# Kernel optimization log

Measured on AMD Instinct MI355X. Metric: run time of the kernel, lower is better.

Reference implementation:

```python
import jax, jax.numpy as jnp
import numpy as np

IN_FEATURES = 4096
OUT_FEATURES = 11008
IN_GROUP = 8
OUT_GROUP = 1
NUM_CODEBOOKS = 1
CODEBOOK_SIZE = 2 ** 16
NUM_OUT_GROUPS = OUT_FEATURES // OUT_GROUP
NUM_IN_GROUPS = IN_FEATURES // IN_GROUP


def setup_inputs() -> dict:
    key = jax.random.key(0)
    k1, k2, k3, k4, k5 = jax.random.split(key, 5)
    x = jax.random.normal(k1, (4, IN_FEATURES), dtype=jnp.float32)
    codebooks = jax.random.normal(k2, (NUM_CODEBOOKS, CODEBOOK_SIZE, OUT_GROUP, IN_GROUP), dtype=jnp.float32)
    codes = jax.random.randint(k3, (NUM_OUT_GROUPS, NUM_IN_GROUPS, NUM_CODEBOOKS), 0, CODEBOOK_SIZE, dtype=jnp.int32)
    scales = jax.random.uniform(k4, (NUM_OUT_GROUPS, 1, 1, 1), dtype=jnp.float32)
    bias = jax.random.normal(k5, (OUT_FEATURES,), dtype=jnp.float32)
    return {"x": x, "codebooks": codebooks, "codes": codes, "scales": scales, "bias": bias}


def _dequantize_weight(codes, codebooks, scales):
    # codes: [Og, Ig, M] int; codebooks: [M, K, og, ig]; scales: [Og,1,1,1]
    m_idx = jnp.arange(codebooks.shape[0])  # [M]
    # advanced indexing: broadcast [M] with [Og,Ig,M] -> gathered [Og,Ig,M,og,ig]
    gathered = codebooks[m_idx[None, None, :], codes]
    w_groups = gathered.sum(axis=2) * scales  # [Og, Ig, og, ig]
    Og, Ig, og, ig = w_groups.shape
    # [Og, og, Ig, ig] -> [Og*og, Ig*ig] = [out_features, in_features]
    return w_groups.transpose(0, 2, 1, 3).reshape(Og * og, Ig * ig)


def reference(x, codebooks, codes, scales, bias):
    weight = _dequantize_weight(codes, codebooks, scales)  # [out, in]
    return x @ weight.T + bias
```

## Files before the change

### kernel.cpp

```cpp
#include <hip/hip_runtime.h>

#define IN_F    4096
#define OUT_F   11008
#define NGROUP  512
#define CHUNK   16
#define NCHUNK  (NGROUP / CHUNK)
#define OTILES  (OUT_F / 256)
#define BATCH   4
#define CBSIZE  65536

typedef int          iv4 __attribute__((ext_vector_type(4)));
typedef unsigned int uv4 __attribute__((ext_vector_type(4)));
typedef float        fv4 __attribute__((ext_vector_type(4)));

__device__ __forceinline__ unsigned bf16rne(float f) {
    unsigned u = __float_as_uint(f);
    return (u + 0x7fffu + ((u >> 16) & 1u)) >> 16;
}
__device__ __forceinline__ float blo(unsigned u) { return __uint_as_float(u << 16); }
__device__ __forceinline__ float bhi(unsigned u) { return __uint_as_float(u & 0xffff0000u); }

__global__ __launch_bounds__(256) void pack_cb_kernel(
    const float* __restrict__ cb, unsigned* __restrict__ cbh)
{
    const int e = blockIdx.x * 256 + threadIdx.x;
    const fv4* src = (const fv4*)(cb + (size_t)e * 8);
    const fv4 a = src[0];
    const fv4 b = src[1];
    uv4 p;
    p.x = bf16rne(a.x) | (bf16rne(a.y) << 16);
    p.y = bf16rne(a.z) | (bf16rne(a.w) << 16);
    p.z = bf16rne(b.x) | (bf16rne(b.y) << 16);
    p.w = bf16rne(b.z) | (bf16rne(b.w) << 16);
    *((uv4*)(cbh + (size_t)e * 4)) = p;
}

__global__ __launch_bounds__(256) void init_out_kernel(
    const float* __restrict__ bias, float* __restrict__ out)
{
    const int o = blockIdx.x * 256 + threadIdx.x;
    out[(size_t)blockIdx.y * OUT_F + o] = bias[o];
}

__global__ __launch_bounds__(256) void aqlm_kernel(
    const float*    __restrict__ x,
    const unsigned* __restrict__ cbh,
    const int*      __restrict__ codes,
    const float*    __restrict__ scales,
    float*          __restrict__ out)
{
    const int o  = blockIdx.x * 256 + threadIdx.x;
    const int g0 = blockIdx.y * CHUNK;

    int code[CHUNK];
    const iv4* cp = (const iv4*)(codes + (size_t)o * NGROUP + g0);
#pragma unroll
    for (int j = 0; j < CHUNK / 4; ++j) {
        const iv4 c = cp[j];
        code[4 * j + 0] = c.x;
        code[4 * j + 1] = c.y;
        code[4 * j + 2] = c.z;
        code[4 * j + 3] = c.w;
    }

    uv4 wq[CHUNK];
#pragma unroll
    for (int j = 0; j < CHUNK; ++j) {
        wq[j] = *((const uv4*)(cbh + (size_t)(unsigned)code[j] * 4u));
    }

    __builtin_amdgcn_sched_barrier(0);

    float acc[BATCH];
#pragma unroll
    for (int b = 0; b < BATCH; ++b) acc[b] = 0.f;

#pragma unroll
    for (int j = 0; j < CHUNK; ++j) {
        const float w0 = blo(wq[j].x), w1 = bhi(wq[j].x);
        const float w2 = blo(wq[j].y), w3 = bhi(wq[j].y);
        const float w4 = blo(wq[j].z), w5 = bhi(wq[j].z);
        const float w6 = blo(wq[j].w), w7 = bhi(wq[j].w);
        const float* xg = x + (size_t)(g0 + j) * 8;
#pragma unroll
        for (int b = 0; b < BATCH; ++b) {
            const float* xb = xg + b * IN_F;
            acc[b] += xb[0] * w0 + xb[1] * w1 + xb[2] * w2 + xb[3] * w3
                    + xb[4] * w4 + xb[5] * w5 + xb[6] * w6 + xb[7] * w7;
        }
    }

    const float s = scales[o];
    atomicAdd(out + 0 * (size_t)OUT_F + o, s * acc[0]);
    atomicAdd(out + 1 * (size_t)OUT_F + o, s * acc[1]);
    atomicAdd(out + 2 * (size_t)OUT_F + o, s * acc[2]);
    atomicAdd(out + 3 * (size_t)OUT_F + o, s * acc[3]);
}

extern "C" void kernel_launch(void* const* d_in, const int* in_sizes, int n_in,
                              void* d_out, int out_size, void* d_ws, size_t ws_size,
                              hipStream_t stream) {
    const float* x      = (const float*)d_in[0];
    const float* cb     = (const float*)d_in[1];
    const int*   codes  = (const int*)d_in[2];
    const float* scales = (const float*)d_in[3];
    const float* bias   = (const float*)d_in[4];
    float* out = (float*)d_out;
    unsigned* cbh = (unsigned*)d_ws;

    hipLaunchKernelGGL(pack_cb_kernel, dim3(CBSIZE / 256), dim3(256), 0, stream,
                       cb, cbh);
    hipLaunchKernelGGL(init_out_kernel, dim3(OTILES, BATCH), dim3(256), 0, stream,
                       bias, out);
    hipLaunchKernelGGL(aqlm_kernel, dim3(OTILES, NCHUNK), dim3(256), 0, stream,
                       x, cbh, codes, scales, out);
}
```

Baseline: 43.85 us.

## Bin codes by codebook slice and serve codebook lookups from LDS

Adds a binning kernel that splits each row's codes into 16 buckets by the high bits of the code. The main kernel then assigns each block one 4096-entry codebook slice, stages that slice and a bf16 copy of x in 96KB of LDS, and accumulates each row's matching bucket entries with half-wave reductions. The aim is to turn random global or L2 codebook gathers into LDS reads. In exchange, code traffic roughly triples (read codes, write buckets, read buckets), a launch is added, and x is rounded to bf16. Any bucket holding more than 96 entries is silently truncated, so correctness depends on codes being spread evenly.

```diff
diff --git a/kernel.cpp b/kernel.cpp
--- a/kernel.cpp
+++ b/kernel.cpp
@@ -1,15 +1,17 @@
 #include <hip/hip_runtime.h>
 
-#define IN_F    4096
-#define OUT_F   11008
-#define NGROUP  512
-#define CHUNK   16
-#define NCHUNK  (NGROUP / CHUNK)
-#define OTILES  (OUT_F / 256)
-#define BATCH   4
-#define CBSIZE  65536
+#define IN_F     4096
+#define OUT_F    11008
+#define NGROUP   512
+#define BATCH    4
+#define CBSIZE   65536
+#define NSLICE   16
+#define SLICE_ENT (CBSIZE / NSLICE)
+#define CAP      96
+#define ROWBLK   16
+#define ROWS_PER_BLOCK (OUT_F / ROWBLK)
+#define OTILES   (OUT_F / 256)
 
-typedef int          iv4 __attribute__((ext_vector_type(4)));
 typedef unsigned int uv4 __attribute__((ext_vector_type(4)));
 typedef float        fv4 __attribute__((ext_vector_type(4)));
 
@@ -42,59 +44,114 @@
     out[(size_t)blockIdx.y * OUT_F + o] = bias[o];
 }
 
-__global__ __launch_bounds__(256) void aqlm_kernel(
+__global__ __launch_bounds__(64) void bin_kernel(
+    const int* __restrict__ codes,
+    unsigned*  __restrict__ buckets,
+    unsigned*  __restrict__ counts)
+{
+    __shared__ unsigned cnt[NSLICE];
+    const int r = blockIdx.x;
+    const int lane = threadIdx.x;
+    if (lane < NSLICE) cnt[lane] = 0;
+    __syncthreads();
+
+    const int* crow = codes + (size_t)r * NGROUP;
+#pragma unroll
+    for (int j = 0; j < NGROUP / 64; ++j) {
+        const int g = j * 64 + lane;
+        const unsigned c = (unsigned)crow[g];
+        const unsigned s = c >> 12;
+        const unsigned e = ((unsigned)g << 12) | (c & 4095u);
+        const unsigned pos = atomicAdd(&cnt[s], 1u);
+        if (pos < CAP)
+            buckets[((size_t)r * NSLICE + s) * CAP + pos] = e;
+    }
+    __syncthreads();
+    if (lane < NSLICE) counts[(size_t)r * NSLICE + lane] = cnt[lane];
+}
+
+__global__ __launch_bounds__(1024) void main_kernel(
     const float*    __restrict__ x,
     const unsigned* __restrict__ cbh,
-    const int*      __restrict__ codes,
+    const unsigned* __restrict__ buckets,
+    const unsigned* __restrict__ counts,
     const float*    __restrict__ scales,
     float*          __restrict__ out)
 {
-    const int o  = blockIdx.x * 256 + threadIdx.x;
-    const int g0 = blockIdx.y * CHUNK;
+    extern __shared__ unsigned lds[];
+    unsigned* cbl = lds;
+    unsigned* xl  = lds + SLICE_ENT * 4;
 
-    int code[CHUNK];
-    const iv4* cp = (const iv4*)(codes + (size_t)o * NGROUP + g0);
-#pragma unroll
-    for (int j = 0; j < CHUNK / 4; ++j) {
-        const iv4 c = cp[j];
-        code[4 * j + 0] = c.x;
-        code[4 * j + 1] = c.y;
-        code[4 * j + 2] = c.z;
-        code[4 * j + 3] = c.w;
+    const int tid = threadIdx.x;
+    const int s   = blockIdx.y;
+
+    {
+        const uv4* src = (const uv4*)cbh + (size_t)s * SLICE_ENT;
+        uv4* dst = (uv4*)cbl;
+        for (int i = tid; i < SLICE_ENT; i += 1024) dst[i] = src[i];
     }
+    for (int i = tid; i < NGROUP * 16; i += 1024) {
+        const int g = i >> 4, b = (i >> 2) & 3, w = i & 3;
+        const float* p = x + (size_t)b * IN_F + g * 8 + w * 2;
+        xl[i] = bf16rne(p[0]) | (bf16rne(p[1]) << 16);
+    }
+    __syncthreads();
 
-    uv4 wq[CHUNK];
-#pragma unroll
-    for (int j = 0; j < CHUNK; ++j) {
-        wq[j] = *((const uv4*)(cbh + (size_t)(unsigned)code[j] * 4u));
-    }
+    const int wave = tid >> 6;
+    const int lane = tid & 63;
+    const int half = lane >> 5;
+    const int l5   = lane & 31;
+    const int rbase = blockIdx.x * ROWS_PER_BLOCK;
 
-    __builtin_amdgcn_sched_barrier(0);
+    for (int it = 0; it < (ROWS_PER_BLOCK + 31) / 32; ++it) {
+        const int  lr    = it * 32 + wave * 2 + half;
+        const bool rowok = lr < ROWS_PER_BLOCK;
+        const int  r     = rbase + (rowok ? lr : 0);
+        unsigned cnt = rowok ? counts[(size_t)r * NSLICE + s] : 0u;
+        if (cnt > CAP) cnt = CAP;
+        const unsigned* brow = buckets + ((size_t)r * NSLICE + s) * CAP;
 
-    float acc[BATCH];
-#pragma unroll
-    for (int b = 0; b < BATCH; ++b) acc[b] = 0.f;
+        float a0 = 0.f, a1 = 0.f, a2 = 0.f, a3 = 0.f;
+        for (unsigned off = (unsigned)l5; ; off += 32) {
+            const bool act = off < cnt;
+            if (__ballot(act) == 0ull) break;
+            if (act) {
+                const unsigned e   = brow[off];
+                const unsigned g   = e >> 12;
+                const unsigned clo = e & 4095u;
+                const uv4 cw = ((const uv4*)cbl)[clo];
+                const uv4 x0 = ((const uv4*)xl)[g * 4 + 0];
+                const uv4 x1 = ((const uv4*)xl)[g * 4 + 1];
+                const uv4 x2 = ((const uv4*)xl)[g * 4 + 2];
+                const uv4 x3 = ((const uv4*)xl)[g * 4 + 3];
+                const float c0 = blo(cw.x), c1 = bhi(cw.x), c2 = blo(cw.y), c3 = bhi(cw.y);
+                const float c4 = blo(cw.z), c5 = bhi(cw.z), c6 = blo(cw.w), c7 = bhi(cw.w);
+                a0 += c0*blo(x0.x) + c1*bhi(x0.x) + c2*blo(x0.y) + c3*bhi(x0.y)
+                    + c4*blo(x0.z) + c5*bhi(x0.z) + c6*blo(x0.w) + c7*bhi(x0.w);
+                a1 += c0*blo(x1.x) + c1*bhi(x1.x) + c2*blo(x1.y) + c3*bhi(x1.y)
+                    + c4*blo(x1.z) + c5*bhi(x1.z) + c6*blo(x1.w) + c7*bhi(x1.w);
+                a2 += c0*blo(x2.x) + c1*bhi(x2.x) + c2*blo(x2.y) + c3*bhi(x2.y)
+                    + c4*blo(x2.z) + c5*bhi(x2.z) + c6*blo(x2.w) + c7*bhi(x2.w);
+                a3 += c0*blo(x3.x) + c1*bhi(x3.x) + c2*blo(x3.y) + c3*bhi(x3.y)
+                    + c4*blo(x3.z) + c5*bhi(x3.z) + c6*blo(x3.w) + c7*bhi(x3.w);
+            }
+        }
 
 #pragma unroll
-    for (int j = 0; j < CHUNK; ++j) {
-        const float w0 = blo(wq[j].x), w1 = bhi(wq[j].x);
-        const float w2 = blo(wq[j].y), w3 = bhi(wq[j].y);
-        const float w4 = blo(wq[j].z), w5 = bhi(wq[j].z);
-        const float w6 = blo(wq[j].w), w7 = bhi(wq[j].w);
-        const float* xg = x + (size_t)(g0 + j) * 8;
-#pragma unroll
-        for (int b = 0; b < BATCH; ++b) {
-            const float* xb = xg + b * IN_F;
-            acc[b] += xb[0] * w0 + xb[1] * w1 + xb[2] * w2 + xb[3] * w3
-                    + xb[4] * w4 + xb[5] * w5 + xb[6] * w6 + xb[7] * w7;
+        for (int m = 16; m >= 1; m >>= 1) {
+            a0 += __shfl_xor(a0, m);
+            a1 += __shfl_xor(a1, m);
+            a2 += __shfl_xor(a2, m);
+            a3 += __shfl_xor(a3, m);
+        }
+        if (l5 == 0 && rowok) {
+            const float sc = scales[r];
+            atomicAdd(out + 0 * (size_t)OUT_F + r, sc * a0);
+            atomicAdd(out + 1 * (size_t)OUT_F + r, sc * a1);
+            atomicAdd(out + 2 * (size_t)OUT_F + r, sc * a2);
+            atomicAdd(out + 3 * (size_t)OUT_F + r, sc * a3);
         }
     }
-
-    const float s = scales[o];
-    atomicAdd(out + 0 * (size_t)OUT_F + o, s * acc[0]);
-    atomicAdd(out + 1 * (size_t)OUT_F + o, s * acc[1]);
-    atomicAdd(out + 2 * (size_t)OUT_F + o, s * acc[2]);
-    atomicAdd(out + 3 * (size_t)OUT_F + o, s * acc[3]);
 }
 
 extern "C" void kernel_launch(void* const* d_in, const int* in_sizes, int n_in,
@@ -106,12 +163,19 @@
     const float* scales = (const float*)d_in[3];
     const float* bias   = (const float*)d_in[4];
     float* out = (float*)d_out;
-    unsigned* cbh = (unsigned*)d_ws;
+
+    unsigned* cbh     = (unsigned*)d_ws;
+    unsigned* buckets = (unsigned*)((char*)d_ws + (1u << 20));
+    unsigned* counts  = (unsigned*)((char*)d_ws + (1u << 20)
+                          + (size_t)OUT_F * NSLICE * CAP * 4u);
 
     hipLaunchKernelGGL(pack_cb_kernel, dim3(CBSIZE / 256), dim3(256), 0, stream,
                        cb, cbh);
+    hipLaunchKernelGGL(bin_kernel, dim3(OUT_F), dim3(64), 0, stream,
+                       codes, buckets, counts);
     hipLaunchKernelGGL(init_out_kernel, dim3(OTILES, BATCH), dim3(256), 0, stream,
                        bias, out);
-    hipLaunchKernelGGL(aqlm_kernel, dim3(OTILES, NCHUNK), dim3(256), 0, stream,
-                       x, cbh, codes, scales, out);
+    hipLaunchKernelGGL(main_kernel, dim3(ROWBLK, NSLICE), dim3(1024),
+                       96 * 1024, stream,
+                       x, cbh, buckets, counts, scales, out);
 }
```

Result: slower. 123.2 us (+181.0%).
